# Kernel tuning notes

Measured on AMD Instinct MI355X. Metric: run time of the kernel, lower is better.

## Reference

```python
import jax, jax.numpy as jnp
import numpy as np

KERNEL_MUL = 2.0
KERNEL_NUM = 5
EPS = 1e-3


def setup_inputs() -> dict:
    key = jax.random.key(0)
    k1, k2 = jax.random.split(key)
    source = jax.random.normal(k1, (2048, 512), dtype=jnp.float32)
    target = jax.random.normal(k2, (2048, 512), dtype=jnp.float32)
    beta = jnp.ones((KERNEL_NUM,), dtype=jnp.float32) / KERNEL_NUM
    return {"source": source, "target": target, "beta": beta}


def _sq_dists(total):
    # squared Euclidean pairwise distances, (N, N), clamped >= 0 (matches cdist(p=2)**2)
    sq = jnp.sum(total * total, axis=-1)
    d = sq[:, None] + sq[None, :] - 2.0 * (total @ total.T)
    return jnp.maximum(d, 0.0)


def _project_simplex(v):
    m = v.shape[0]
    mu = -jnp.sort(-v)                      # descending
    cs = jnp.cumsum(mu)
    ar = jnp.arange(1, m + 1, dtype=v.dtype)
    cond = mu - (cs - 1.0) / ar > 0
    idx = jnp.where(cond, jnp.arange(m), -1)
    rho = jnp.where(jnp.any(cond), jnp.max(idx), 0)
    theta = (cs[rho] - 1.0) / (rho + 1).astype(v.dtype)
    p = jnp.maximum(v - theta, 0.0)
    return p / (p.sum() + 1e-12)


def _update_beta(source, target, beta):
    # Batched version of the per-pair quad-kernel loop in _update_beta.
    Ns, D = source.shape
    Nt = target.shape[0]
    P = min(Ns // 2, Nt // 2)  # num_effective_pairs (static)
    s = source[: 2 * P].reshape(P, 2, D)
    t = target[: 2 * P].reshape(P, 2, D)
    quad = jnp.concatenate([s, t], axis=1)              # (P, 4, D) -> [s1, s2, t1, t2]
    diff = quad[:, :, None, :] - quad[:, None, :, :]
    sq = jnp.sum(diff * diff, axis=-1)                  # (P, 4, 4)
    offdiag = ~np.eye(4, dtype=bool)
    bw = jnp.median(sq[:, offdiag], axis=1) + 1e-6      # per-pair median of nonzero dists
    bw = bw / (KERNEL_MUL ** (KERNEL_NUM // 2))
    bws = bw[:, None] * (KERNEL_MUL ** jnp.arange(KERNEL_NUM, dtype=bw.dtype))[None, :]
    K = jnp.exp(-sq[:, None, :, :] / bws[:, :, None, None])   # (P, 5, 4, 4)
    g = K[:, :, 0, 1] + K[:, :, 2, 3] - K[:, :, 0, 2] - K[:, :, 1, 3]  # (P, 5)
    gm = jnp.mean(g, axis=0)
    Q = (g.T @ g) / P - jnp.outer(gm, gm) + EPS * jnp.eye(KERNEL_NUM, dtype=g.dtype)
    # projected gradient descent on the simplex (lr=1, max_iter=100, tol=1e-6)
    def cond_fn(st):
        _, _, i, conv = st
        return (i < 100) & (~conv)
    def body_fn(st):
        b, _, i, _ = st
        proj = _project_simplex(b - Q @ b)
        conv = jnp.linalg.norm(proj - b) < 1e-6
        return (proj, proj, i + 1, conv)
    _, proj, _, _ = jax.lax.while_loop(
        cond_fn, body_fn, (beta, beta, jnp.int32(0), jnp.array(False)))
    return proj


def _forward(source, target, beta):
    beta_new = _update_beta(jax.lax.stop_gradient(source),
                            jax.lax.stop_gradient(target), beta)
    Ns = source.shape[0]
    total = jnp.concatenate([source, target], axis=0)   # (N, D)
    N = total.shape[0]
    sq = _sq_dists(total)                               # (N, N)
    offdiag = ~np.eye(N, dtype=bool)
    bw = jnp.median(sq[offdiag]) + 1e-6
    bw = bw / (KERNEL_MUL ** (KERNEL_NUM // 2))
    bws = bw * (KERNEL_MUL ** jnp.arange(KERNEL_NUM, dtype=sq.dtype))  # (5,)
    Ks = jnp.exp(-sq[None, :, :] / bws[:, None, None])  # (5, N, N)
    joint = jnp.einsum('k,kij->ij', beta_new, Ks)
    XX = joint[:Ns, :Ns]
    YY = joint[Ns:, Ns:]
    XY = joint[:Ns, Ns:]
    n = XX.shape[0]
    m = YY.shape[0]
    term_XX = (jnp.sum(XX) - jnp.trace(XX)) / (n * (n - 1))
    term_YY = (jnp.sum(YY) - jnp.trace(YY)) / (m * (m - 1))
    term_XY = jnp.sum(XY) / (n * m)
    loss = term_XX + term_YY - 2.0 * term_XY
    return jnp.maximum(loss, 0.0)


def reference(source, target, beta):
    return _forward(source, target, beta)
```

## Files before the change

kernel.cpp:

```cpp
#include <hip/hip_runtime.h>
#include <math.h>

#define NT 4096
#define NS 2048
#define DDIM 512
#define KN 5
#define NTILES 528
#define RANKA 8386559u
#define RANKB 8386560u

typedef __bf16 bf16x8 __attribute__((ext_vector_type(8)));
typedef float f32x4 __attribute__((ext_vector_type(4)));
typedef unsigned short u16x8 __attribute__((ext_vector_type(8)));

static __device__ inline unsigned short f2bf(float x) {
    unsigned u = __float_as_uint(x);
    unsigned r = (u + 0x7fffu + ((u >> 16) & 1u)) >> 16;
    return (unsigned short)r;
}
static __device__ inline float bf2f(unsigned short h) {
    return __uint_as_float(((unsigned)h) << 16);
}

static __device__ inline void tri_map(int b, int& bx, int& by) {
    int x = (int)((sqrtf(8.0f * (float)b + 1.0f) - 1.0f) * 0.5f);
    while ((x + 1) * (x + 2) / 2 <= b) ++x;
    while (x * (x + 1) / 2 > b) --x;
    bx = x;
    by = b - x * (x + 1) / 2;
}

static __device__ inline void wscan(const unsigned* __restrict__ h, int C, unsigned r,
                                    unsigned& bin, unsigned& rem)
{
    int lane = threadIdx.x;
    unsigned s = 0;
    for (int i = 0; i < C; ++i) s += h[lane * C + i];
    unsigned x = s;
    #pragma unroll
    for (int off = 1; off < 64; off <<= 1) {
        unsigned y = __shfl_up(x, off);
        if (lane >= off) x += y;
    }
    unsigned base = x - s;
    bool has = (r >= base) && (r < base + s);
    unsigned long long mm = __ballot(has);
    int leader = __ffsll(mm) - 1;
    unsigned b = 0, cb = 0;
    if (lane == leader) {
        unsigned cc = base;
        for (int i = 0; i < C; ++i) {
            unsigned hv = h[lane * C + i];
            if (r < cc + hv) { b = lane * C + i; cb = cc; break; }
            cc += hv;
        }
    }
    bin = __shfl(b, leader);
    rem = r - __shfl(cb, leader);
}

static __device__ void beta_solve(const float* __restrict__ g,
                                  const float* __restrict__ beta_in,
                                  float* __restrict__ beta_out)
{
    int lane = threadIdx.x;
    float gs[KN] = {0, 0, 0, 0, 0};
    float gg[15];
    #pragma unroll
    for (int i = 0; i < 15; ++i) gg[i] = 0.0f;
    for (int p = lane; p < 1024; p += 64) {
        float gv[KN];
        #pragma unroll
        for (int k = 0; k < KN; ++k) gv[k] = g[(size_t)p * KN + k];
        int idx = 0;
        #pragma unroll
        for (int a2 = 0; a2 < KN; ++a2) {
            gs[a2] += gv[a2];
            #pragma unroll
            for (int b2 = a2; b2 < KN; ++b2) gg[idx++] += gv[a2] * gv[b2];
        }
    }
    #pragma unroll
    for (int m = 32; m > 0; m >>= 1) {
        #pragma unroll
        for (int k = 0; k < KN; ++k) gs[k] += __shfl_xor(gs[k], m);
        #pragma unroll
        for (int i = 0; i < 15; ++i) gg[i] += __shfl_xor(gg[i], m);
    }
    if (lane != 0) return;

    float Q[KN][KN], gm[KN];
    #pragma unroll
    for (int k = 0; k < KN; ++k) gm[k] = gs[k] * (1.0f / 1024.0f);
    int idx = 0;
    #pragma unroll
    for (int a2 = 0; a2 < KN; ++a2)
        #pragma unroll
        for (int b2 = a2; b2 < KN; ++b2) {
            float qv = gg[idx++] * (1.0f / 1024.0f) - gm[a2] * gm[b2];
            Q[a2][b2] = qv; Q[b2][a2] = qv;
        }
    #pragma unroll
    for (int k = 0; k < KN; ++k) Q[k][k] += 0.001f;

    float b[KN], proj[KN];
    #pragma unroll
    for (int k = 0; k < KN; ++k) { b[k] = beta_in[k]; proj[k] = b[k]; }
    for (int it = 0; it < 100; ++it) {
        float v[KN];
        #pragma unroll
        for (int a2 = 0; a2 < KN; ++a2) {
            float qb = Q[a2][0] * b[0] + Q[a2][1] * b[1] + Q[a2][2] * b[2]
                     + Q[a2][3] * b[3] + Q[a2][4] * b[4];
            v[a2] = b[a2] - qb;
        }
        float mu0 = v[0], mu1 = v[1], mu2 = v[2], mu3 = v[3], mu4 = v[4];
#define CMPSW(x, y) { float hi_ = fmaxf(x, y); float lo_ = fminf(x, y); x = hi_; y = lo_; }
        CMPSW(mu0, mu1) CMPSW(mu3, mu4) CMPSW(mu2, mu4) CMPSW(mu2, mu3)
        CMPSW(mu0, mu3) CMPSW(mu0, mu2) CMPSW(mu1, mu4) CMPSW(mu1, mu3) CMPSW(mu1, mu2)
#undef CMPSW
        float cs0 = mu0, cs1 = cs0 + mu1, cs2 = cs1 + mu2, cs3 = cs2 + mu3, cs4 = cs3 + mu4;
        bool c1 = mu1 * 2.0f > cs1 - 1.0f;
        bool c2 = mu2 * 3.0f > cs2 - 1.0f;
        bool c3 = mu3 * 4.0f > cs3 - 1.0f;
        bool c4 = mu4 * 5.0f > cs4 - 1.0f;
        float csSel = cs0, rcpSel = 1.0f;
        if (c1) { csSel = cs1; rcpSel = 0.5f; }
        if (c2) { csSel = cs2; rcpSel = (1.0f / 3.0f); }
        if (c3) { csSel = cs3; rcpSel = 0.25f; }
        if (c4) { csSel = cs4; rcpSel = 0.2f; }
        float theta = (csSel - 1.0f) * rcpSel;
        float ssum = 0.0f;
        #pragma unroll
        for (int k = 0; k < KN; ++k) { proj[k] = fmaxf(v[k] - theta, 0.0f); ssum += proj[k]; }
        float invs = 1.0f / (ssum + 1e-12f);
        float nd = 0.0f;
        #pragma unroll
        for (int k = 0; k < KN; ++k) {
            proj[k] *= invs;
            float dd = proj[k] - b[k];
            nd += dd * dd;
            b[k] = proj[k];
        }
        if (nd < 1e-12f) break;
    }
    #pragma unroll
    for (int k = 0; k < KN; ++k) beta_out[k] = proj[k];
}

__global__ __launch_bounds__(256) void k_prep2(const float* __restrict__ S,
                                               const float* __restrict__ T,
                                               unsigned short* __restrict__ Hi,
                                               unsigned short* __restrict__ Lo,
                                               float* __restrict__ norms,
                                               float* __restrict__ g,
                                               unsigned* __restrict__ hists)
{
    if (blockIdx.x < 45) hists[blockIdx.x * 256 + threadIdx.x] = 0;
    int p = blockIdx.x * 4 + (threadIdx.x >> 6);
    int l = threadIdx.x & 63;
    const float* r0 = S + (size_t)(2 * p) * DDIM;
    const float* r1 = r0 + DDIM;
    const float* r2 = T + (size_t)(2 * p) * DDIM;
    const float* r3 = r2 + DDIM;
    float a[8], b[8], c[8], d[8];
    *(float4*)&a[0] = *(const float4*)(r0 + l * 8); *(float4*)&a[4] = *(const float4*)(r0 + l * 8 + 4);
    *(float4*)&b[0] = *(const float4*)(r1 + l * 8); *(float4*)&b[4] = *(const float4*)(r1 + l * 8 + 4);
    *(float4*)&c[0] = *(const float4*)(r2 + l * 8); *(float4*)&c[4] = *(const float4*)(r2 + l * 8 + 4);
    *(float4*)&d[0] = *(const float4*)(r3 + l * 8); *(float4*)&d[4] = *(const float4*)(r3 + l * 8 + 4);

    float n0 = 0, n1 = 0, n2 = 0, n3 = 0;
    float s01 = 0, s23 = 0, s02 = 0, s13 = 0, s03 = 0, s12 = 0;
    u16x8 h0, l0, h1, l1, h2, l2, h3, l3;
    #pragma unroll
    for (int k = 0; k < 8; ++k) {
        float va = a[k], vb = b[k], vc = c[k], vd = d[k];
        n0 += va * va; n1 += vb * vb; n2 += vc * vc; n3 += vd * vd;
        float t01 = va - vb, t23 = vc - vd, t02 = va - vc, t13 = vb - vd;
        s01 += t01*t01; s23 += t23*t23; s02 += t02*t02; s13 += t13*t13;
        float t03 = va - vd, t12 = vb - vc;
        s03 += t03*t03; s12 += t12*t12;
        unsigned short hh;
        hh = f2bf(va); h0[k] = hh; l0[k] = f2bf(va - bf2f(hh));
        hh = f2bf(vb); h1[k] = hh; l1[k] = f2bf(vb - bf2f(hh));
        hh = f2bf(vc); h2[k] = hh; l2[k] = f2bf(vc - bf2f(hh));
        hh = f2bf(vd); h3[k] = hh; l3[k] = f2bf(vd - bf2f(hh));
    }
    size_t g0 = (size_t)(2 * p) * DDIM + l * 8;
    size_t g1 = g0 + DDIM;
    size_t g2 = (size_t)(NS + 2 * p) * DDIM + l * 8;
    size_t g3 = g2 + DDIM;
    *(u16x8*)&Hi[g0] = h0; *(u16x8*)&Lo[g0] = l0;
    *(u16x8*)&Hi[g1] = h1; *(u16x8*)&Lo[g1] = l1;
    *(u16x8*)&Hi[g2] = h2; *(u16x8*)&Lo[g2] = l2;
    *(u16x8*)&Hi[g3] = h3; *(u16x8*)&Lo[g3] = l3;

    #pragma unroll
    for (int m = 32; m > 0; m >>= 1) {
        n0 += __shfl_xor(n0, m); n1 += __shfl_xor(n1, m);
        n2 += __shfl_xor(n2, m); n3 += __shfl_xor(n3, m);
        s01 += __shfl_xor(s01, m); s23 += __shfl_xor(s23, m);
        s02 += __shfl_xor(s02, m); s13 += __shfl_xor(s13, m);
        s03 += __shfl_xor(s03, m); s12 += __shfl_xor(s12, m);
    }
    if (l == 0) {
        norms[2 * p] = n0; norms[2 * p + 1] = n1;
        norms[NS + 2 * p] = n2; norms[NS + 2 * p + 1] = n3;
        float v[6] = { s01, s02, s03, s12, s13, s23 };
        for (int i = 0; i < 5; ++i)
            for (int j = 0; j < 5 - i; ++j)
                if (v[j] > v[j + 1]) { float t = v[j]; v[j] = v[j + 1]; v[j + 1] = t; }
        float med = 0.5f * (v[2] + v[3]);
        float bw = (med + 1e-6f) * 0.25f;
        #pragma unroll
        for (int k = 0; k < KN; ++k) {
            float inv = 1.0f / (bw * (float)(1 << k));
            g[(size_t)p * KN + k] = expf(-s01 * inv) + expf(-s23 * inv)
                                  - expf(-s02 * inv) - expf(-s13 * inv);
        }
    }
}

__global__ __launch_bounds__(256) void k_dist_mfma(const unsigned short* __restrict__ Hi,
                                                   const unsigned short* __restrict__ Lo,
                                                   const float* __restrict__ norms,
                                                   float* __restrict__ D,
                                                   const float* __restrict__ g,
                                                   const float* __restrict__ beta_in,
                                                   float* __restrict__ beta_out,
                                                   unsigned* __restrict__ gH)
{
    __shared__ __align__(16) unsigned short sA[2][2][128][32];
    __shared__ __align__(16) unsigned short sB[2][2][128][32];

    if (blockIdx.x == 0) {
        if (threadIdx.x < 64) beta_solve(g, beta_in, beta_out);
        return;
    }

    int bb = blockIdx.x - 1;
    int swz = (bb & 7) * 66 + (bb >> 3);
    int bx, by;
    tri_map(swz, bx, by);
    const int m0 = by * 128, n0 = bx * 128;

    const int tid = threadIdx.x;
    const int w = tid >> 6, l = tid & 63;
    const int wr = w >> 1, wc = w & 1;

    const int chunk = (l & 3) ^ ((((l >> 2) & 3) + ((l >> 4) & 3)) & 3);
    const size_t gA0 = (size_t)(m0 + w * 16 + (l >> 2)) * DDIM + chunk * 8;
    const size_t gA1 = gA0 + (size_t)64 * DDIM;
    const size_t gB0 = (size_t)(n0 + w * 16 + (l >> 2)) * DDIM + chunk * 8;
    const size_t gB1 = gB0 + (size_t)64 * DDIM;
    const unsigned w1024 = w * 1024;

#define GLD(dst, srcptr, goff)                                                      \
    __builtin_amdgcn_global_load_lds(                                               \
        (const __attribute__((address_space(1))) unsigned*)((srcptr) + (goff)),     \
        (__attribute__((address_space(3))) unsigned*)((char*)(dst) + w1024), 16, 0, 0)
#define STAGE(buf, kk)                                  \
    do {                                                \
        GLD(&sA[buf][0][0][0],  Hi, gA0 + (kk));        \
        GLD(&sA[buf][0][64][0], Hi, gA1 + (kk));        \
        GLD(&sA[buf][1][0][0],  Lo, gA0 + (kk));        \
        GLD(&sA[buf][1][64][0], Lo, gA1 + (kk));        \
        GLD(&sB[buf][0][0][0],  Hi, gB0 + (kk));        \
        GLD(&sB[buf][0][64][0], Hi, gB1 + (kk));        \
        GLD(&sB[buf][1][0][0],  Lo, gB0 + (kk));        \
        GLD(&sB[buf][1][64][0], Lo, gB1 + (kk));        \
    } while (0)

    f32x4 acc[4][4] = {};
    const int q = l >> 4;
    const int fr = ((l & 3) + ((l >> 2) & 3)) & 3;
    const unsigned soff = ((unsigned)(q ^ fr)) << 4;
    const unsigned rowbA = (wr * 64 + (l & 15)) * 64 + soff;
    const unsigned rowbB = (wc * 64 + (l & 15)) * 64 + soff;

    STAGE(0, 0);
    __syncthreads();

    #pragma unroll 2
    for (int t = 0; t < 16; ++t) {
        const int cur = t & 1;
        if (t < 15) STAGE(cur ^ 1, (t + 1) * 32);

        bf16x8 ah[4], al[4], bh[4], bl[4];
        #pragma unroll
        for (int m = 0; m < 4; ++m) {
            ah[m] = *(const bf16x8*)((const char*)&sA[cur][0][0][0] + rowbA + m * 1024);
            al[m] = *(const bf16x8*)((const char*)&sA[cur][1][0][0] + rowbA + m * 1024);
        }
        #pragma unroll
        for (int n = 0; n < 4; ++n) {
            bh[n] = *(const bf16x8*)((const char*)&sB[cur][0][0][0] + rowbB + n * 1024);
            bl[n] = *(const bf16x8*)((const char*)&sB[cur][1][0][0] + rowbB + n * 1024);
        }
        #pragma unroll
        for (int m = 0; m < 4; ++m)
            #pragma unroll
            for (int n = 0; n < 4; ++n) {
                acc[m][n] = __builtin_amdgcn_mfma_f32_16x16x32_bf16(bh[n], ah[m], acc[m][n], 0, 0, 0);
                acc[m][n] = __builtin_amdgcn_mfma_f32_16x16x32_bf16(bl[n], ah[m], acc[m][n], 0, 0, 0);
                acc[m][n] = __builtin_amdgcn_mfma_f32_16x16x32_bf16(bh[n], al[m], acc[m][n], 0, 0, 0);
            }
        __syncthreads();
    }
#undef STAGE
#undef GLD

    float* ncache = (float*)&sB[0][0][0][0];
    unsigned* hrep = (unsigned*)&sB[0][0][0][0] + 256;
    if (tid < 128) ncache[tid] = norms[m0 + tid];
    else           ncache[tid] = norms[n0 + tid - 128];
    for (int i = tid; i < 4096; i += 256) hrep[i] = 0;
    __syncthreads();

    unsigned* hmine = hrep + w * 1024;
    const unsigned wgt = (bx != by) ? 2u : 1u;
    float* rowbuf = (float*)&sA[0][0][0][0] + w * 1024;
    const int rr = l & 15;
    #pragma unroll
    for (int m = 0; m < 4; ++m) {
        float nrm = ncache[wr * 64 + m * 16 + rr];
        #pragma unroll
        for (int n = 0; n < 4; ++n) {
            float4 ncv = *(const float4*)&ncache[128 + wc * 64 + n * 16 + (q << 2)];
            f32x4 a = acc[m][n];
            float4 o;
            o.x = fmaxf(nrm + ncv.x - 2.0f * a[0], 0.0f);
            o.y = fmaxf(nrm + ncv.y - 2.0f * a[1], 0.0f);
            o.z = fmaxf(nrm + ncv.z - 2.0f * a[2], 0.0f);
            o.w = fmaxf(nrm + ncv.w - 2.0f * a[3], 0.0f);
            int ch = (n * 4 + q) ^ (rr & 7);
            *(float4*)(rowbuf + rr * 64 + ch * 4) = o;
        }
        #pragma unroll
        for (int s = 0; s < 4; ++s) {
            int row = s * 4 + q;
            int ch = (l & 15) ^ (row & 7);
            float4 v = *(const float4*)(rowbuf + row * 64 + ch * 4);
            int rowg = m0 + wr * 64 + m * 16 + row;
            int colg = n0 + wc * 64 + (l & 15) * 4;
            *(float4*)&D[(size_t)rowg * NT + colg] = v;
            unsigned b0_ = __float_as_uint(v.x) >> 22;
            unsigned b1_ = __float_as_uint(v.y) >> 22;
            unsigned b2_ = __float_as_uint(v.z) >> 22;
            unsigned b3_ = __float_as_uint(v.w) >> 22;
            unsigned pb = b0_, pc = (rowg == colg) ? 0u : wgt;
            unsigned cj;
            cj = (rowg == colg + 1) ? 0u : wgt;
            if (b1_ == pb) pc += cj; else { if (pc) atomicAdd(&hmine[pb], pc); pb = b1_; pc = cj; }
            cj = (rowg == colg + 2) ? 0u : wgt;
            if (b2_ == pb) pc += cj; else { if (pc) atomicAdd(&hmine[pb], pc); pb = b2_; pc = cj; }
            cj = (rowg == colg + 3) ? 0u : wgt;
            if (b3_ == pb) pc += cj; else { if (pc) atomicAdd(&hmine[pb], pc); pb = b3_; pc = cj; }
            if (pc) atomicAdd(&hmine[pb], pc);
        }
    }
    __syncthreads();
    for (int i = tid; i < 1024; i += 256) {
        unsigned c = hrep[i] + hrep[i + 1024] + hrep[i + 2048] + hrep[i + 3072];
        if (c) atomicAdd(&gH[i], c);
    }
}

__global__ __launch_bounds__(256) void k_h1(const float* __restrict__ D,
                                            const unsigned* __restrict__ gH,
                                            unsigned* __restrict__ g1A,
                                            unsigned* __restrict__ g1B)
{
    __shared__ unsigned lha[1024];
    __shared__ unsigned lhb[1024];
    __shared__ unsigned sres[2];
    int tid = threadIdx.x;
    for (int i = tid; i < 1024; i += 256) { lha[i] = 0; lhb[i] = 0; }
    if (tid < 64) {
        unsigned pA, remA, pB, remB;
        wscan(gH, 16, RANKA, pA, remA);
        wscan(gH, 16, RANKB, pB, remB);
        if (tid == 0) { sres[0] = pA; sres[1] = pB; }
    }
    __syncthreads();
    unsigned pA = sres[0], pB = sres[1];
    int bx, by;
    tri_map(blockIdx.x, bx, by);
    int m0 = by * 128, n0 = bx * 128;
    unsigned wt = (bx != by) ? 2u : 1u;
    for (int v = tid; v < 4096; v += 256) {
        int r = m0 + (v >> 5);
        int c0 = n0 + (v & 31) * 4;
        float4 dv = *(const float4*)&D[(size_t)r * NT + c0];
        const float* dd = (const float*)&dv;
        #pragma unroll
        for (int j = 0; j < 4; ++j) {
            if (r == c0 + j) continue;
            unsigned key = __float_as_uint(dd[j]);
            if ((key >> 22) == pA) atomicAdd(&lha[(key >> 12) & 1023], wt);
            if ((key >> 22) == pB) atomicAdd(&lhb[(key >> 12) & 1023], wt);
        }
    }
    __syncthreads();
    for (int i = tid; i < 1024; i += 256) {
        unsigned ca = lha[i];
        if (ca) atomicAdd(&g1A[i], ca);
        unsigned cb = lhb[i];
        if (cb) atomicAdd(&g1B[i], cb);
    }
}

__global__ __launch_bounds__(256) void k_h2(const float* __restrict__ D,
                                            const unsigned* __restrict__ gH,
                                            const unsigned* __restrict__ g1A,
                                            const unsigned* __restrict__ g1B,
                                            unsigned* __restrict__ g2A,
                                            unsigned* __restrict__ g2B)
{
    __shared__ unsigned lha[4096];
    __shared__ unsigned lhb[4096];
    __shared__ unsigned sres[2];
    int tid = threadIdx.x;
    for (int i = tid; i < 4096; i += 256) { lha[i] = 0; lhb[i] = 0; }
    if (tid < 64) {
        unsigned pA, remA, pB, remB, b1A, r1A, b1B, r1B;
        wscan(gH, 16, RANKA, pA, remA);
        wscan(gH, 16, RANKB, pB, remB);
        wscan(g1A, 16, remA, b1A, r1A);
        wscan(g1B, 16, remB, b1B, r1B);
        if (tid == 0) { sres[0] = (pA << 10) | b1A; sres[1] = (pB << 10) | b1B; }
    }
    __syncthreads();
    unsigned preA = sres[0], preB = sres[1];
    int bx, by;
    tri_map(blockIdx.x, bx, by);
    int m0 = by * 128, n0 = bx * 128;
    unsigned wt = (bx != by) ? 2u : 1u;
    for (int v = tid; v < 4096; v += 256) {
        int r = m0 + (v >> 5);
        int c0 = n0 + (v & 31) * 4;
        float4 dv = *(const float4*)&D[(size_t)r * NT + c0];
        const float* dd = (const float*)&dv;
        #pragma unroll
        for (int j = 0; j < 4; ++j) {
            if (r == c0 + j) continue;
            unsigned key = __float_as_uint(dd[j]);
            if ((key >> 12) == preA) atomicAdd(&lha[key & 4095], wt);
            if ((key >> 12) == preB) atomicAdd(&lhb[key & 4095], wt);
        }
    }
    __syncthreads();
    for (int i = tid; i < 4096; i += 256) {
        unsigned ca = lha[i];
        if (ca) atomicAdd(&g2A[i], ca);
        unsigned cb = lhb[i];
        if (cb) atomicAdd(&g2B[i], cb);
    }
}

__global__ __launch_bounds__(256) void k_wsumf(const float* __restrict__ D,
                                               const unsigned* __restrict__ gH,
                                               const unsigned* __restrict__ g1A,
                                               const unsigned* __restrict__ g1B,
                                               const unsigned* __restrict__ g2A,
                                               const unsigned* __restrict__ g2B,
                                               const float* __restrict__ beta,
                                               double* __restrict__ partials,
                                               unsigned* __restrict__ cnt,
                                               float* __restrict__ out)
{
    __shared__ double red[256];
    __shared__ unsigned sres[2];
    __shared__ unsigned tk;
    int tid = threadIdx.x;
    if (tid < 64) {
        unsigned pA, remA, pB, remB, b1A, r1A, b1B, r1B, b2A, r2A, b2B, r2B;
        wscan(gH, 16, RANKA, pA, remA);
        wscan(gH, 16, RANKB, pB, remB);
        wscan(g1A, 16, remA, b1A, r1A);
        wscan(g1B, 16, remB, b1B, r1B);
        wscan(g2A, 64, r1A, b2A, r2A);
        wscan(g2B, 64, r1B, b2B, r2B);
        if (tid == 0) {
            sres[0] = (((pA << 10) | b1A) << 12) | b2A;
            sres[1] = (((pB << 10) | b1B) << 12) | b2B;
        }
    }
    __syncthreads();
    float med = 0.5f * (__uint_as_float(sres[0]) + __uint_as_float(sres[1]));
    float bw = (med + 1e-6f) * 0.25f;
    float i0 = 1.0f / (bw * 1.0f);
    float i1 = 1.0f / (bw * 2.0f);
    float i2 = 1.0f / (bw * 4.0f);
    float i3 = 1.0f / (bw * 8.0f);
    float i4 = 1.0f / (bw * 16.0f);
    float b0 = beta[0], b1 = beta[1], b2 = beta[2], b3 = beta[3], b4 = beta[4];
    const double wDiag = 1.0 / ((double)NS * (NS - 1));
    const double wOff = -1.0 / ((double)NS * NS);
    int bx, by;
    tri_map(blockIdx.x, bx, by);
    int m0 = by * 128, n0 = bx * 128;
    double wt = (bx != by) ? 2.0 : 1.0;
    double acc = 0.0;
    for (int v = tid; v < 4096; v += 256) {
        int r = m0 + (v >> 5);
        int c0 = n0 + (v & 31) * 4;
        float4 dv = *(const float4*)&D[(size_t)r * NT + c0];
        const float* dd = (const float*)&dv;
        #pragma unroll
        for (int j = 0; j < 4; ++j) {
            int c = c0 + j;
            if (r == c) continue;
            float sq = dd[j];
            float val = b0 * __expf(-sq * i0) + b1 * __expf(-sq * i1) + b2 * __expf(-sq * i2)
                      + b3 * __expf(-sq * i3) + b4 * __expf(-sq * i4);
            bool same = (r < NS) == (c < NS);
            acc += (same ? wDiag : wOff) * (double)val;
        }
    }
    acc *= wt;
    red[tid] = acc;
    __syncthreads();
    for (int off = 128; off > 0; off >>= 1) {
        if (tid < off) red[tid] += red[tid + off];
        __syncthreads();
    }
    if (tid == 0) {
        partials[blockIdx.x] = red[0];
        __threadfence();
        tk = atomicAdd(&cnt[0], 1u);
    }
    __syncthreads();
    if (tk == NTILES - 1) {
        __threadfence();
        double a2 = 0.0;
        for (int i = tid; i < NTILES; i += 256) {
            unsigned long long u = atomicAdd((unsigned long long*)&partials[i], 0ull);
            a2 += __longlong_as_double(u);
        }
        red[tid] = a2;
        __syncthreads();
        for (int off = 128; off > 0; off >>= 1) {
            if (tid < off) red[tid] += red[tid + off];
            __syncthreads();
        }
        if (tid == 0) out[0] = (float)fmax(red[0], 0.0);
    }
}

extern "C" void kernel_launch(void* const* d_in, const int* in_sizes, int n_in,
                              void* d_out, int out_size, void* d_ws, size_t ws_size,
                              hipStream_t stream)
{
    const float* S = (const float*)d_in[0];
    const float* T = (const float*)d_in[1];
    const float* beta = (const float*)d_in[2];
    float* out = (float*)d_out;

    float* D = (float*)d_ws;
    unsigned short* Hi = (unsigned short*)(D + (size_t)NT * NT);
    unsigned short* Lo = Hi + (size_t)NT * DDIM;
    float* norms = (float*)(Lo + (size_t)NT * DDIM);
    float* g = norms + NT;
    float* beta2 = g + 1024 * KN;
    unsigned* hists = (unsigned*)(beta2 + 8);
    unsigned* hL0 = hists;
    unsigned* g1A = hists + 1024;
    unsigned* g1B = hists + 2048;
    unsigned* g2A = hists + 3072;
    unsigned* g2B = hists + 7168;
    unsigned* cnt = hists + 11264;
    double* partials = (double*)(hists + 11520);

    k_prep2<<<dim3(256), dim3(256), 0, stream>>>(S, T, Hi, Lo, norms, g, hists);
    k_dist_mfma<<<dim3(NTILES + 1), dim3(256), 0, stream>>>(Hi, Lo, norms, D, g, beta, beta2, hL0);
    k_h1<<<dim3(NTILES), dim3(256), 0, stream>>>(D, hL0, g1A, g1B);
    k_h2<<<dim3(NTILES), dim3(256), 0, stream>>>(D, hL0, g1A, g1B, g2A, g2B);
    k_wsumf<<<dim3(NTILES), dim3(256), 0, stream>>>(D, hL0, g1A, g1B, g2A, g2B,
                                                    beta2, partials, cnt, out);
}
```

Before: 156.6 us.

## Merge histogram-select passes into one persistent kernel with grid barriers

The coarse histogram moves out of the distance-GEMM epilogue, and the three radix-select passes plus the weighted-sum pass are merged into one persistent kernel. A leader block computes the selected bins between passes, and global atomic counters act as grid barriers, which removes several kernel launches and repeated prefix scans. The five exponentials are replaced by one exp followed by repeated squaring, since the bandwidths are powers of two. In exchange the merged kernel relies on all 529 blocks being co-resident, or the spin-waits deadlock or time out, and it rereads D from global memory in every pass.

```diff
diff --git a/kernel.cpp b/kernel.cpp
--- a/kernel.cpp
+++ b/kernel.cpp
@@ -6,8 +6,7 @@
 #define DDIM 512
 #define KN 5
 #define NTILES 528
-#define RANKA 8386559u
-#define RANKB 8386560u
+#define NBLK 529
 
 typedef __bf16 bf16x8 __attribute__((ext_vector_type(8)));
 typedef float f32x4 __attribute__((ext_vector_type(4)));
@@ -29,6 +28,11 @@
     bx = x;
     by = b - x * (x + 1) / 2;
 }
+static __device__ inline int xcd_tile(int bb) {
+    return (bb & 7) * 66 + (bb >> 3);
+}
+
+static __device__ inline unsigned aload(unsigned* p) { return atomicAdd(p, 0u); }
 
 static __device__ inline void wscan(const unsigned* __restrict__ h, int C, unsigned r,
                                     unsigned& bin, unsigned& rem)
@@ -154,9 +158,15 @@
                                                unsigned short* __restrict__ Lo,
                                                float* __restrict__ norms,
                                                float* __restrict__ g,
-                                               unsigned* __restrict__ hists)
+                                               unsigned* __restrict__ hists,
+                                               unsigned* __restrict__ sel)
 {
     if (blockIdx.x < 45) hists[blockIdx.x * 256 + threadIdx.x] = 0;
+    if (blockIdx.x == 50 && threadIdx.x == 0) {
+        sel[0] = 0u; sel[1] = 8386559u;
+        sel[2] = 0u; sel[3] = 8386560u;
+        sel[4] = 0u;
+    }
     int p = blockIdx.x * 4 + (threadIdx.x >> 6);
     int l = threadIdx.x & 63;
     const float* r0 = S + (size_t)(2 * p) * DDIM;
@@ -227,8 +237,7 @@
                                                    float* __restrict__ D,
                                                    const float* __restrict__ g,
                                                    const float* __restrict__ beta_in,
-                                                   float* __restrict__ beta_out,
-                                                   unsigned* __restrict__ gH)
+                                                   float* __restrict__ beta_out)
 {
     __shared__ __align__(16) unsigned short sA[2][2][128][32];
     __shared__ __align__(16) unsigned short sB[2][2][128][32];
@@ -238,10 +247,8 @@
         return;
     }
 
-    int bb = blockIdx.x - 1;
-    int swz = (bb & 7) * 66 + (bb >> 3);
     int bx, by;
-    tri_map(swz, bx, by);
+    tri_map(xcd_tile(blockIdx.x - 1), bx, by);
     const int m0 = by * 128, n0 = bx * 128;
 
     const int tid = threadIdx.x;
@@ -311,14 +318,10 @@
 #undef GLD
 
     float* ncache = (float*)&sB[0][0][0][0];
-    unsigned* hrep = (unsigned*)&sB[0][0][0][0] + 256;
     if (tid < 128) ncache[tid] = norms[m0 + tid];
     else           ncache[tid] = norms[n0 + tid - 128];
-    for (int i = tid; i < 4096; i += 256) hrep[i] = 0;
     __syncthreads();
 
-    unsigned* hmine = hrep + w * 1024;
-    const unsigned wgt = (bx != by) ? 2u : 1u;
     float* rowbuf = (float*)&sA[0][0][0][0] + w * 1024;
     const int rr = l & 15;
     #pragma unroll
@@ -341,211 +344,270 @@
             int row = s * 4 + q;
             int ch = (l & 15) ^ (row & 7);
             float4 v = *(const float4*)(rowbuf + row * 64 + ch * 4);
-            int rowg = m0 + wr * 64 + m * 16 + row;
-            int colg = n0 + wc * 64 + (l & 15) * 4;
-            *(float4*)&D[(size_t)rowg * NT + colg] = v;
-            unsigned b0_ = __float_as_uint(v.x) >> 22;
-            unsigned b1_ = __float_as_uint(v.y) >> 22;
-            unsigned b2_ = __float_as_uint(v.z) >> 22;
-            unsigned b3_ = __float_as_uint(v.w) >> 22;
-            unsigned pb = b0_, pc = (rowg == colg) ? 0u : wgt;
-            unsigned cj;
-            cj = (rowg == colg + 1) ? 0u : wgt;
-            if (b1_ == pb) pc += cj; else { if (pc) atomicAdd(&hmine[pb], pc); pb = b1_; pc = cj; }
-            cj = (rowg == colg + 2) ? 0u : wgt;
-            if (b2_ == pb) pc += cj; else { if (pc) atomicAdd(&hmine[pb], pc); pb = b2_; pc = cj; }
-            cj = (rowg == colg + 3) ? 0u : wgt;
-            if (b3_ == pb) pc += cj; else { if (pc) atomicAdd(&hmine[pb], pc); pb = b3_; pc = cj; }
-            if (pc) atomicAdd(&hmine[pb], pc);
-        }
-    }
-    __syncthreads();
-    for (int i = tid; i < 1024; i += 256) {
-        unsigned c = hrep[i] + hrep[i + 1024] + hrep[i + 2048] + hrep[i + 3072];
-        if (c) atomicAdd(&gH[i], c);
-    }
-}
-
-__global__ __launch_bounds__(256) void k_h1(const float* __restrict__ D,
-                                            const unsigned* __restrict__ gH,
-                                            unsigned* __restrict__ g1A,
-                                            unsigned* __restrict__ g1B)
+            *(float4*)&D[(size_t)(m0 + wr * 64 + m * 16 + row) * NT + n0 + wc * 64 + (l & 15) * 4] = v;
+        }
+    }
+}
+
+__global__ __launch_bounds__(256) void k_msel(const float* __restrict__ D,
+                                              unsigned* __restrict__ sel,
+                                              unsigned* __restrict__ gH,
+                                              unsigned* __restrict__ g1A,
+                                              unsigned* __restrict__ g1B,
+                                              unsigned* __restrict__ g2A,
+                                              unsigned* __restrict__ g2B,
+                                              unsigned* __restrict__ cnt,
+                                              const float* __restrict__ beta,
+                                              double* __restrict__ partials,
+                                              float* __restrict__ out)
 {
-    __shared__ unsigned lha[1024];
-    __shared__ unsigned lhb[1024];
-    __shared__ unsigned sres[2];
-    int tid = threadIdx.x;
-    for (int i = tid; i < 1024; i += 256) { lha[i] = 0; lhb[i] = 0; }
-    if (tid < 64) {
-        unsigned pA, remA, pB, remB;
-        wscan(gH, 16, RANKA, pA, remA);
-        wscan(gH, 16, RANKB, pB, remB);
-        if (tid == 0) { sres[0] = pA; sres[1] = pB; }
-    }
-    __syncthreads();
-    unsigned pA = sres[0], pB = sres[1];
-    int bx, by;
-    tri_map(blockIdx.x, bx, by);
-    int m0 = by * 128, n0 = bx * 128;
-    unsigned wt = (bx != by) ? 2u : 1u;
-    for (int v = tid; v < 4096; v += 256) {
-        int r = m0 + (v >> 5);
-        int c0 = n0 + (v & 31) * 4;
-        float4 dv = *(const float4*)&D[(size_t)r * NT + c0];
-        const float* dd = (const float*)&dv;
-        #pragma unroll
-        for (int j = 0; j < 4; ++j) {
-            if (r == c0 + j) continue;
-            unsigned key = __float_as_uint(dd[j]);
-            if ((key >> 22) == pA) atomicAdd(&lha[(key >> 12) & 1023], wt);
-            if ((key >> 22) == pB) atomicAdd(&lhb[(key >> 12) & 1023], wt);
-        }
-    }
-    __syncthreads();
-    for (int i = tid; i < 1024; i += 256) {
-        unsigned ca = lha[i];
-        if (ca) atomicAdd(&g1A[i], ca);
-        unsigned cb = lhb[i];
-        if (cb) atomicAdd(&g1B[i], cb);
-    }
-}
-
-__global__ __launch_bounds__(256) void k_h2(const float* __restrict__ D,
-                                            const unsigned* __restrict__ gH,
-                                            const unsigned* __restrict__ g1A,
-                                            const unsigned* __restrict__ g1B,
-                                            unsigned* __restrict__ g2A,
-                                            unsigned* __restrict__ g2B)
-{
-    __shared__ unsigned lha[4096];
-    __shared__ unsigned lhb[4096];
-    __shared__ unsigned sres[2];
-    int tid = threadIdx.x;
-    for (int i = tid; i < 4096; i += 256) { lha[i] = 0; lhb[i] = 0; }
-    if (tid < 64) {
-        unsigned pA, remA, pB, remB, b1A, r1A, b1B, r1B;
-        wscan(gH, 16, RANKA, pA, remA);
-        wscan(gH, 16, RANKB, pB, remB);
-        wscan(g1A, 16, remA, b1A, r1A);
-        wscan(g1B, 16, remB, b1B, r1B);
-        if (tid == 0) { sres[0] = (pA << 10) | b1A; sres[1] = (pB << 10) | b1B; }
-    }
-    __syncthreads();
-    unsigned preA = sres[0], preB = sres[1];
-    int bx, by;
-    tri_map(blockIdx.x, bx, by);
-    int m0 = by * 128, n0 = bx * 128;
-    unsigned wt = (bx != by) ? 2u : 1u;
-    for (int v = tid; v < 4096; v += 256) {
-        int r = m0 + (v >> 5);
-        int c0 = n0 + (v & 31) * 4;
-        float4 dv = *(const float4*)&D[(size_t)r * NT + c0];
-        const float* dd = (const float*)&dv;
-        #pragma unroll
-        for (int j = 0; j < 4; ++j) {
-            if (r == c0 + j) continue;
-            unsigned key = __float_as_uint(dd[j]);
-            if ((key >> 12) == preA) atomicAdd(&lha[key & 4095], wt);
-            if ((key >> 12) == preB) atomicAdd(&lhb[key & 4095], wt);
-        }
-    }
-    __syncthreads();
-    for (int i = tid; i < 4096; i += 256) {
-        unsigned ca = lha[i];
-        if (ca) atomicAdd(&g2A[i], ca);
-        unsigned cb = lhb[i];
-        if (cb) atomicAdd(&g2B[i], cb);
-    }
-}
-
-__global__ __launch_bounds__(256) void k_wsumf(const float* __restrict__ D,
-                                               const unsigned* __restrict__ gH,
-                                               const unsigned* __restrict__ g1A,
-                                               const unsigned* __restrict__ g1B,
-                                               const unsigned* __restrict__ g2A,
-                                               const unsigned* __restrict__ g2B,
-                                               const float* __restrict__ beta,
-                                               double* __restrict__ partials,
-                                               unsigned* __restrict__ cnt,
-                                               float* __restrict__ out)
-{
+    __shared__ unsigned lds[8192];
     __shared__ double red[256];
-    __shared__ unsigned sres[2];
     __shared__ unsigned tk;
-    int tid = threadIdx.x;
-    if (tid < 64) {
-        unsigned pA, remA, pB, remB, b1A, r1A, b1B, r1B, b2A, r2A, b2B, r2B;
-        wscan(gH, 16, RANKA, pA, remA);
-        wscan(gH, 16, RANKB, pB, remB);
-        wscan(g1A, 16, remA, b1A, r1A);
-        wscan(g1B, 16, remB, b1B, r1B);
-        wscan(g2A, 64, r1A, b2A, r2A);
-        wscan(g2B, 64, r1B, b2B, r2B);
-        if (tid == 0) {
-            sres[0] = (((pA << 10) | b1A) << 12) | b2A;
-            sres[1] = (((pB << 10) | b1B) << 12) | b2B;
-        }
-    }
-    __syncthreads();
-    float med = 0.5f * (__uint_as_float(sres[0]) + __uint_as_float(sres[1]));
-    float bw = (med + 1e-6f) * 0.25f;
-    float i0 = 1.0f / (bw * 1.0f);
-    float i1 = 1.0f / (bw * 2.0f);
-    float i2 = 1.0f / (bw * 4.0f);
-    float i3 = 1.0f / (bw * 8.0f);
-    float i4 = 1.0f / (bw * 16.0f);
-    float b0 = beta[0], b1 = beta[1], b2 = beta[2], b3 = beta[3], b4 = beta[4];
-    const double wDiag = 1.0 / ((double)NS * (NS - 1));
-    const double wOff = -1.0 / ((double)NS * NS);
-    int bx, by;
-    tri_map(blockIdx.x, bx, by);
-    int m0 = by * 128, n0 = bx * 128;
-    double wt = (bx != by) ? 2.0 : 1.0;
-    double acc = 0.0;
-    for (int v = tid; v < 4096; v += 256) {
-        int r = m0 + (v >> 5);
-        int c0 = n0 + (v & 31) * 4;
-        float4 dv = *(const float4*)&D[(size_t)r * NT + c0];
-        const float* dd = (const float*)&dv;
-        #pragma unroll
-        for (int j = 0; j < 4; ++j) {
-            int c = c0 + j;
-            if (r == c) continue;
-            float sq = dd[j];
-            float val = b0 * __expf(-sq * i0) + b1 * __expf(-sq * i1) + b2 * __expf(-sq * i2)
-                      + b3 * __expf(-sq * i3) + b4 * __expf(-sq * i4);
-            bool same = (r < NS) == (c < NS);
-            acc += (same ? wDiag : wOff) * (double)val;
-        }
-    }
-    acc *= wt;
-    red[tid] = acc;
-    __syncthreads();
-    for (int off = 128; off > 0; off >>= 1) {
-        if (tid < off) red[tid] += red[tid + off];
-        __syncthreads();
-    }
-    if (tid == 0) {
-        partials[blockIdx.x] = red[0];
+    const int tid = threadIdx.x;
+    const bool lead = (blockIdx.x == 0);
+    int m0 = 0, n0 = 0;
+    unsigned wt = 1;
+    bool diagT = false;
+    if (!lead) {
+        int bx, by;
+        tri_map(xcd_tile(blockIdx.x - 1), bx, by);
+        m0 = by * 128; n0 = bx * 128;
+        wt = (bx != by) ? 2u : 1u;
+        diagT = (bx == by);
+    }
+    (void)diagT;
+
+#define ARRIVE(K) do { __threadfence(); __syncthreads(); \
+        if (tid == 0) atomicAdd(&cnt[K], 1u); } while (0)
+#define WAITFOR(K, VAL) do { if (tid == 0) { unsigned it_ = 0; \
+        while (atomicAdd(&cnt[K], 0u) < (VAL)) { \
+            __builtin_amdgcn_s_sleep(8); if (++it_ > 100000000u) break; } } \
+        __syncthreads(); } while (0)
+
+    if (!lead) {
+        for (int i = tid; i < 1024; i += 256) lds[i] = 0;
+        __syncthreads();
+        #pragma unroll
+        for (int i = 0; i < 16; ++i) {
+            int v = tid + 256 * i;
+            int r = m0 + (v >> 5), c0 = n0 + (v & 31) * 4;
+            float4 dv = *(const float4*)&D[(size_t)r * NT + c0];
+            const float* dd = (const float*)&dv;
+            unsigned pb = __float_as_uint(dd[0]) >> 22;
+            unsigned pc = (r == c0) ? 0u : wt;
+            #pragma unroll
+            for (int j = 1; j < 4; ++j) {
+                unsigned bj = __float_as_uint(dd[j]) >> 22;
+                unsigned cj = (r == c0 + j) ? 0u : wt;
+                if (bj == pb) pc += cj;
+                else { if (pc) atomicAdd(&lds[pb], pc); pb = bj; pc = cj; }
+            }
+            if (pc) atomicAdd(&lds[pb], pc);
+        }
+        __syncthreads();
+        for (int i = tid; i < 1024; i += 256) {
+            unsigned c = lds[i];
+            if (c) atomicAdd(&gH[i], c);
+        }
+    }
+    ARRIVE(0);
+    if (lead) {
+        WAITFOR(0, NBLK);
+        for (int i = tid; i < 1024; i += 256) lds[i] = aload(&gH[i]);
+        __syncthreads();
+        if (tid < 64) {
+            unsigned bA, rA, bB, rB;
+            wscan(lds, 16, 8386559u, bA, rA);
+            wscan(lds, 16, 8386560u, bB, rB);
+            if (tid == 0) {
+                atomicExch(&sel[0], bA); atomicExch(&sel[1], rA);
+                atomicExch(&sel[2], bB); atomicExch(&sel[3], rB);
+            }
+        }
         __threadfence();
-        tk = atomicAdd(&cnt[0], 1u);
-    }
-    __syncthreads();
-    if (tk == NTILES - 1) {
+        __syncthreads();
+        if (tid == 0) atomicAdd(&cnt[0], 1u);
+    } else {
+        WAITFOR(0, NBLK + 1);
+    }
+
+    if (!lead) {
+        unsigned pA, pB;
+        if (tid == 0) { lds[8190] = aload(&sel[0]); lds[8191] = aload(&sel[2]); }
+        for (int i = tid; i < 2048; i += 256) lds[i] = 0;
+        __syncthreads();
+        pA = lds[8190]; pB = lds[8191];
+        #pragma unroll
+        for (int i = 0; i < 16; ++i) {
+            int v = tid + 256 * i;
+            int r = m0 + (v >> 5), c0 = n0 + (v & 31) * 4;
+            float4 dv = *(const float4*)&D[(size_t)r * NT + c0];
+            const float* dd = (const float*)&dv;
+            #pragma unroll
+            for (int j = 0; j < 4; ++j) {
+                if (r == c0 + j) continue;
+                unsigned key = __float_as_uint(dd[j]);
+                if ((key >> 22) == pA) atomicAdd(&lds[(key >> 12) & 1023], wt);
+                if ((key >> 22) == pB) atomicAdd(&lds[1024 + ((key >> 12) & 1023)], wt);
+            }
+        }
+        __syncthreads();
+        for (int i = tid; i < 1024; i += 256) {
+            unsigned ca = lds[i];
+            if (ca) atomicAdd(&g1A[i], ca);
+            unsigned cb = lds[1024 + i];
+            if (cb) atomicAdd(&g1B[i], cb);
+        }
+    }
+    ARRIVE(1);
+    if (lead) {
+        WAITFOR(1, NBLK);
+        for (int i = tid; i < 1024; i += 256) {
+            lds[i] = aload(&g1A[i]);
+            lds[1024 + i] = aload(&g1B[i]);
+        }
+        __syncthreads();
+        if (tid < 64) {
+            unsigned pA = aload(&sel[0]), rkA = aload(&sel[1]);
+            unsigned pB = aload(&sel[2]), rkB = aload(&sel[3]);
+            unsigned bA, rA, bB, rB;
+            wscan(lds, 16, rkA, bA, rA);
+            wscan(lds + 1024, 16, rkB, bB, rB);
+            if (tid == 0) {
+                atomicExch(&sel[0], (pA << 10) | bA); atomicExch(&sel[1], rA);
+                atomicExch(&sel[2], (pB << 10) | bB); atomicExch(&sel[3], rB);
+            }
+        }
         __threadfence();
-        double a2 = 0.0;
-        for (int i = tid; i < NTILES; i += 256) {
-            unsigned long long u = atomicAdd((unsigned long long*)&partials[i], 0ull);
-            a2 += __longlong_as_double(u);
-        }
-        red[tid] = a2;
+        __syncthreads();
+        if (tid == 0) atomicAdd(&cnt[1], 1u);
+    } else {
+        WAITFOR(1, NBLK + 1);
+    }
+
+    if (!lead) {
+        unsigned pA, pB;
+        if (tid == 0) { unsigned a = aload(&sel[0]), b = aload(&sel[2]); lds[0] = a; lds[1] = b; }
+        __syncthreads();
+        pA = lds[0]; pB = lds[1];
+        __syncthreads();
+        for (int i = tid; i < 8192; i += 256) lds[i] = 0;
+        __syncthreads();
+        #pragma unroll
+        for (int i = 0; i < 16; ++i) {
+            int v = tid + 256 * i;
+            int r = m0 + (v >> 5), c0 = n0 + (v & 31) * 4;
+            float4 dv = *(const float4*)&D[(size_t)r * NT + c0];
+            const float* dd = (const float*)&dv;
+            #pragma unroll
+            for (int j = 0; j < 4; ++j) {
+                if (r == c0 + j) continue;
+                unsigned key = __float_as_uint(dd[j]);
+                if ((key >> 12) == pA) atomicAdd(&lds[key & 4095], wt);
+                if ((key >> 12) == pB) atomicAdd(&lds[4096 + (key & 4095)], wt);
+            }
+        }
+        __syncthreads();
+        for (int i = tid; i < 4096; i += 256) {
+            unsigned ca = lds[i];
+            if (ca) atomicAdd(&g2A[i], ca);
+            unsigned cb = lds[4096 + i];
+            if (cb) atomicAdd(&g2B[i], cb);
+        }
+    }
+    ARRIVE(2);
+    if (lead) {
+        WAITFOR(2, NBLK);
+        for (int i = tid; i < 4096; i += 256) {
+            lds[i] = aload(&g2A[i]);
+            lds[4096 + i] = aload(&g2B[i]);
+        }
+        __syncthreads();
+        if (tid < 64) {
+            unsigned pA = aload(&sel[0]), rkA = aload(&sel[1]);
+            unsigned pB = aload(&sel[2]), rkB = aload(&sel[3]);
+            unsigned bA, rA, bB, rB;
+            wscan(lds, 64, rkA, bA, rA);
+            wscan(lds + 4096, 64, rkB, bB, rB);
+            if (tid == 0) {
+                unsigned keyA = (pA << 12) | bA;
+                unsigned keyB = (pB << 12) | bB;
+                float med = 0.5f * (__uint_as_float(keyA) + __uint_as_float(keyB));
+                float bw = (med + 1e-6f) * 0.25f;
+                float i4 = 1.0f / (bw * 16.0f);
+                atomicExch(&sel[4], __float_as_uint(i4));
+            }
+        }
+        __threadfence();
+        __syncthreads();
+        if (tid == 0) atomicAdd(&cnt[2], 1u);
+        return;
+    } else {
+        WAITFOR(2, NBLK + 1);
+    }
+
+    {
+        if (tid == 0) lds[0] = aload(&sel[4]);
+        __syncthreads();
+        float i4 = __uint_as_float(lds[0]);
+        float b0 = beta[0], b1 = beta[1], b2 = beta[2], b3 = beta[3], b4 = beta[4];
+        const double wDiag = 1.0 / ((double)NS * (NS - 1));
+        const double wOff = -1.0 / ((double)NS * NS);
+        double wtd = (wt == 2u) ? 2.0 : 1.0;
+        double acc = 0.0;
+        #pragma unroll
+        for (int i = 0; i < 16; ++i) {
+            int v = tid + 256 * i;
+            int r = m0 + (v >> 5), c0 = n0 + (v & 31) * 4;
+            float4 dv = *(const float4*)&D[(size_t)r * NT + c0];
+            const float* dd = (const float*)&dv;
+            #pragma unroll
+            for (int j = 0; j < 4; ++j) {
+                int c = c0 + j;
+                if (r == c) continue;
+                float sq = dd[j];
+                float y1 = __expf(-sq * i4);
+                float y2 = y1 * y1;
+                float y4 = y2 * y2;
+                float y8 = y4 * y4;
+                float y16 = y8 * y8;
+                float val = b4 * y1 + b3 * y2 + b2 * y4 + b1 * y8 + b0 * y16;
+                bool same = (r < NS) == (c < NS);
+                acc += (same ? wDiag : wOff) * (double)val;
+            }
+        }
+        acc *= wtd;
+        red[tid] = acc;
         __syncthreads();
         for (int off = 128; off > 0; off >>= 1) {
             if (tid < off) red[tid] += red[tid + off];
             __syncthreads();
         }
-        if (tid == 0) out[0] = (float)fmax(red[0], 0.0);
-    }
+        if (tid == 0) {
+            partials[blockIdx.x - 1] = red[0];
+            __threadfence();
+            tk = atomicAdd(&cnt[3], 1u);
+        }
+        __syncthreads();
+        if (tk == NTILES - 1) {
+            __threadfence();
+            double a2 = 0.0;
+            for (int i = tid; i < NTILES; i += 256) {
+                unsigned long long u = atomicAdd((unsigned long long*)&partials[i], 0ull);
+                a2 += __longlong_as_double(u);
+            }
+            red[tid] = a2;
+            __syncthreads();
+            for (int off = 128; off > 0; off >>= 1) {
+                if (tid < off) red[tid] += red[tid + off];
+                __syncthreads();
+            }
+            if (tid == 0) out[0] = (float)fmax(red[0], 0.0);
+        }
+    }
+#undef ARRIVE
+#undef WAITFOR
 }
 
 extern "C" void kernel_launch(void* const* d_in, const int* in_sizes, int n_in,
@@ -563,8 +625,9 @@
     float* norms = (float*)(Lo + (size_t)NT * DDIM);
     float* g = norms + NT;
     float* beta2 = g + 1024 * KN;
-    unsigned* hists = (unsigned*)(beta2 + 8);
-    unsigned* hL0 = hists;
+    unsigned* sel = (unsigned*)(beta2 + 8);
+    unsigned* hists = sel + 16;
+    unsigned* gH  = hists;
     unsigned* g1A = hists + 1024;
     unsigned* g1B = hists + 2048;
     unsigned* g2A = hists + 3072;
@@ -572,10 +635,8 @@
     unsigned* cnt = hists + 11264;
     double* partials = (double*)(hists + 11520);
 
-    k_prep2<<<dim3(256), dim3(256), 0, stream>>>(S, T, Hi, Lo, norms, g, hists);
-    k_dist_mfma<<<dim3(NTILES + 1), dim3(256), 0, stream>>>(Hi, Lo, norms, D, g, beta, beta2, hL0);
-    k_h1<<<dim3(NTILES), dim3(256), 0, stream>>>(D, hL0, g1A, g1B);
-    k_h2<<<dim3(NTILES), dim3(256), 0, stream>>>(D, hL0, g1A, g1B, g2A, g2B);
-    k_wsumf<<<dim3(NTILES), dim3(256), 0, stream>>>(D, hL0, g1A, g1B, g2A, g2B,
-                                                    beta2, partials, cnt, out);
-}
+    k_prep2<<<dim3(256), dim3(256), 0, stream>>>(S, T, Hi, Lo, norms, g, hists, sel);
+    k_dist_mfma<<<dim3(NTILES + 1), dim3(256), 0, stream>>>(Hi, Lo, norms, D, g, beta, beta2);
+    k_msel<<<dim3(NBLK), dim3(256), 0, stream>>>(D, sel, gH, g1A, g1B, g2A, g2B,
+                                                 cnt, beta2, partials, out);
+}
```

Result: slower. 319.2 us (+103.8%).
